# Performance work log

Hardware: AMD Instinct MI355X
Metric: run time of the kernel (lower is better)

## Reference

```python
import jax, jax.numpy as jnp
import numpy as np

D_MODEL = 512
NUM_HEADS = 8
DEPTH = D_MODEL // NUM_HEADS
B, S = 8, 1024


def setup_inputs() -> dict:
    key = jax.random.key(0)
    ks = jax.random.split(key, 14)
    scale = 1.0 / np.sqrt(D_MODEL)
    inp = {
        "q_in": jax.random.normal(ks[0], (B, S, D_MODEL), jnp.float32),
        "k_in": jax.random.normal(ks[1], (B, S, D_MODEL), jnp.float32),
        "v_in": jax.random.normal(ks[2], (B, S, D_MODEL), jnp.float32),
        # padding mask: 1 = masked-out position
        "mask": jax.random.randint(ks[3], (B, 1, 1, S), 0, 2).astype(jnp.float32),
        "additional_weights": jax.random.uniform(ks[4], (B, S, S), jnp.float32),
        "wq": jax.random.normal(ks[5], (D_MODEL, D_MODEL), jnp.float32) * scale,
        "bq": jnp.zeros((D_MODEL,), jnp.float32),
        "wk": jax.random.normal(ks[6], (D_MODEL, D_MODEL), jnp.float32) * scale,
        "bk": jnp.zeros((D_MODEL,), jnp.float32),
        "wv": jax.random.normal(ks[7], (D_MODEL, D_MODEL), jnp.float32) * scale,
        "bv": jnp.zeros((D_MODEL,), jnp.float32),
        "wo": jax.random.normal(ks[8], (D_MODEL, D_MODEL), jnp.float32) * scale,
        "bo": jnp.zeros((D_MODEL,), jnp.float32),
    }
    return inp


def _split_heads(x):
    # [B, S, d_model] -> [B, H, S, depth]
    b, s, _ = x.shape
    return x.reshape(b, s, NUM_HEADS, DEPTH).transpose(0, 2, 1, 3)


def reference(q_in, k_in, v_in, mask, additional_weights,
              wq, bq, wk, bk, wv, bv, wo, bo):
    q = _split_heads(q_in @ wq + bq)  # [B,H,S,D]
    k = _split_heads(k_in @ wk + bk)
    v = _split_heads(v_in @ wv + bv)

    scores = jnp.einsum("bhqd,bhkd->bhqk", q, k) / jnp.sqrt(
        jnp.asarray(DEPTH, q.dtype))
    scores = scores + mask * -1e9
    attn = jax.nn.softmax(scores, axis=-1)
    # post-softmax multiplicative weights, broadcast over heads
    attn = attn * additional_weights[:, None, :, :]
    x = jnp.einsum("bhqk,bhkd->bhqd", attn, v)
    x = x.transpose(0, 2, 1, 3).reshape(q_in.shape[0], -1, D_MODEL)
    out = x @ wo + bo
    return out, attn
```

## Files before the change

kernel.cpp:

```cpp
#include <hip/hip_runtime.h>
#include <stdint.h>

typedef unsigned short u16;
typedef short bf16x8 __attribute__((ext_vector_type(8)));
typedef float f32x4 __attribute__((ext_vector_type(4)));
typedef u16 u16x8 __attribute__((ext_vector_type(8)));

#define NHEADS 8
#define SEQ 1024
#define DM 512
#define DEPTH 64
#define BATCH 8
#define PSTRIDE 1032

__device__ __forceinline__ u16 f2bf(float f) {
    union { float f; unsigned u; } v; v.f = f;
    unsigned r = v.u + 0x7FFF + ((v.u >> 16) & 1);
    return (u16)(r >> 16);
}

__global__ void __launch_bounds__(256) transpose512(
    const float* __restrict__ w0, const float* __restrict__ w1,
    const float* __restrict__ w2, const float* __restrict__ w3,
    u16* __restrict__ wt)
{
    __shared__ float tile[32][33];
    const float* w = (blockIdx.z == 0) ? w0 : (blockIdx.z == 1) ? w1
                   : (blockIdx.z == 2) ? w2 : w3;
    u16* o = wt + (size_t)blockIdx.z * (DM * DM);
    int rb = blockIdx.y * 32, cb = blockIdx.x * 32;
    int tx = threadIdx.x, ty = threadIdx.y;
    #pragma unroll
    for (int k = 0; k < 32; k += 8)
        tile[ty + k][tx] = w[(size_t)(rb + ty + k) * DM + cb + tx];
    __syncthreads();
    #pragma unroll
    for (int k = 0; k < 32; k += 8)
        o[(size_t)(cb + ty + k) * DM + rb + tx] = f2bf(tile[tx][ty + k]);
}

__global__ void __launch_bounds__(256) conv_bf16(
    const float* __restrict__ q, const float* __restrict__ k,
    const float* __restrict__ v,
    u16* __restrict__ oq, u16* __restrict__ ok, u16* __restrict__ ov)
{
    const float* src = (blockIdx.z == 0) ? q : (blockIdx.z == 1) ? k : v;
    u16* dst = (blockIdx.z == 0) ? oq : (blockIdx.z == 1) ? ok : ov;
    size_t i = ((size_t)blockIdx.x * 256 + threadIdx.x) * 8;
    f32x4 a = *(const f32x4*)(src + i);
    f32x4 b = *(const f32x4*)(src + i + 4);
    u16x8 o;
    #pragma unroll
    for (int j = 0; j < 4; j++) { o[j] = f2bf(a[j]); o[j + 4] = f2bf(b[j]); }
    *(u16x8*)(dst + i) = o;
}

template <int LAYOUT>
__device__ __forceinline__ void gemm_tile(
    const u16* __restrict__ A, const u16* __restrict__ wt,
    const float* __restrict__ bias, void* __restrict__ out_)
{
    const int tid = threadIdx.x;
    const int wid = tid >> 6, lane = tid & 63;
    const int wm = wid >> 1, wn = wid & 1;
    const int mb = blockIdx.y * 128 + wm * 64;
    const int nb = blockIdx.x * 128 + wn * 64;
    const int lr = lane & 15, g = lane >> 4, lk = g * 8;

    f32x4 acc[4][4];
    #pragma unroll
    for (int i = 0; i < 4; i++)
        #pragma unroll
        for (int j = 0; j < 4; j++) acc[i][j] = (f32x4)0.f;

    for (int ks = 0; ks < DM; ks += 32) {
        bf16x8 a[4], bf[4];
        #pragma unroll
        for (int mt = 0; mt < 4; mt++)
            a[mt] = *(const bf16x8*)(A + (size_t)(mb + mt * 16 + lr) * DM + ks + lk);
        #pragma unroll
        for (int nt = 0; nt < 4; nt++)
            bf[nt] = *(const bf16x8*)(wt + (size_t)(nb + nt * 16 + lr) * DM + ks + lk);
        #pragma unroll
        for (int mt = 0; mt < 4; mt++)
            #pragma unroll
            for (int nt = 0; nt < 4; nt++) {
                if (LAYOUT == 1)
                    acc[mt][nt] = __builtin_amdgcn_mfma_f32_16x16x32_bf16(
                        bf[nt], a[mt], acc[mt][nt], 0, 0, 0);
                else
                    acc[mt][nt] = __builtin_amdgcn_mfma_f32_16x16x32_bf16(
                        a[mt], bf[nt], acc[mt][nt], 0, 0, 0);
            }
    }

    #pragma unroll
    for (int mt = 0; mt < 4; mt++) {
        #pragma unroll
        for (int nt = 0; nt < 4; nt++) {
            #pragma unroll
            for (int r = 0; r < 4; r++) {
                if (LAYOUT == 1) {
                    int m = mb + mt * 16 + lr;
                    int n = nb + nt * 16 + 4 * g + r;
                    float val = acc[mt][nt][r] + bias[n];
                    int b_ = m >> 10, s = m & 1023, h = n >> 6, d = n & 63;
                    ((u16*)out_)[((size_t)((b_ * NHEADS + h) << 6) + d) * SEQ + s] = f2bf(val);
                } else {
                    int n = nb + nt * 16 + lr;
                    int m = mb + mt * 16 + 4 * g + r;
                    float val = acc[mt][nt][r] + bias[n];
                    if (LAYOUT == 2) {
                        ((float*)out_)[(size_t)m * DM + n] = val;
                    } else {
                        int b_ = m >> 10, s = m & 1023, h = n >> 6, d = n & 63;
                        ((u16*)out_)[(((size_t)(b_ * NHEADS + h) * SEQ + s) << 6) + d] = f2bf(val);
                    }
                }
            }
        }
    }
}

__global__ void __launch_bounds__(256) qkv_proj(
    const u16* __restrict__ qbf, const u16* __restrict__ kbf,
    const u16* __restrict__ vbf, const u16* __restrict__ wt_base,
    const float* __restrict__ bq, const float* __restrict__ bk,
    const float* __restrict__ bv,
    u16* __restrict__ Qb, u16* __restrict__ Kb, u16* __restrict__ VTb)
{
    int z = blockIdx.z;
    if (z == 0)      gemm_tile<0>(qbf, wt_base,               bq, Qb);
    else if (z == 1) gemm_tile<0>(kbf, wt_base + DM * DM,     bk, Kb);
    else             gemm_tile<1>(vbf, wt_base + 2 * DM * DM, bv, VTb);
}

__global__ void __launch_bounds__(256) out_proj(
    const u16* __restrict__ X, const u16* __restrict__ wto,
    const float* __restrict__ bo, float* __restrict__ out)
{
    gemm_tile<2>(X, wto, bo, out);
}

__global__ void __launch_bounds__(256) attn_kernel(
    const u16* __restrict__ Q, const u16* __restrict__ K,
    const u16* __restrict__ VT, const float* __restrict__ mask,
    const float* __restrict__ addw, float* __restrict__ attn_out,
    u16* __restrict__ X)
{
    __shared__ u16 Pl[16 * PSTRIDE];
    __shared__ float redm[4][16];
    __shared__ float reds[4][16];
    const int h = blockIdx.x, qt = blockIdx.y, b = blockIdx.z;
    const int tid = threadIdx.x, wid = tid >> 6, lane = tid & 63;
    const int lr = lane & 15, g = lane >> 4, lk = g * 8;
    const size_t head = (size_t)(b * NHEADS + h) * (SEQ * DEPTH);
    const u16* Qh = Q + head + (size_t)qt * 16 * DEPTH;
    const u16* Kh = K + head;
    const u16* Vh = VT + head;
    const int cbase = (wid << 8) + lr;

    bf16x8 af0 = *(const bf16x8*)(Qh + lr * DEPTH + lk);
    bf16x8 af1 = *(const bf16x8*)(Qh + lr * DEPTH + 32 + lk);
    f32x4 acc[16];
    #pragma unroll
    for (int nt = 0; nt < 16; nt++) acc[nt] = (f32x4)0.f;
    #pragma unroll
    for (int nt = 0; nt < 16; nt++) {
        const u16* kp = Kh + (size_t)(cbase + (nt << 4)) * DEPTH + lk;
        bf16x8 b0 = *(const bf16x8*)kp;
        bf16x8 b1 = *(const bf16x8*)(kp + 32);
        acc[nt] = __builtin_amdgcn_mfma_f32_16x16x32_bf16(af0, b0, acc[nt], 0, 0, 0);
        acc[nt] = __builtin_amdgcn_mfma_f32_16x16x32_bf16(af1, b1, acc[nt], 0, 0, 0);
    }

    const float* mrow = mask + ((size_t)b << 10);
    float mx[4];
    #pragma unroll
    for (int r = 0; r < 4; r++) mx[r] = -3.0e38f;
    #pragma unroll
    for (int nt = 0; nt < 16; nt++) {
        float mp = mrow[cbase + (nt << 4)] * -1e9f;
        #pragma unroll
        for (int r = 0; r < 4; r++) {
            acc[nt][r] = acc[nt][r] * 0.125f + mp;
            mx[r] = fmaxf(mx[r], acc[nt][r]);
        }
    }
    #pragma unroll
    for (int off = 1; off < 16; off <<= 1)
        #pragma unroll
        for (int r = 0; r < 4; r++)
            mx[r] = fmaxf(mx[r], __shfl_xor(mx[r], off, 64));
    if (lr < 4)
        redm[wid][4 * g + lr] = (lr == 0) ? mx[0] : (lr == 1) ? mx[1]
                              : (lr == 2) ? mx[2] : mx[3];
    __syncthreads();
    float gm[4];
    #pragma unroll
    for (int r = 0; r < 4; r++)
        gm[r] = fmaxf(fmaxf(redm[0][4 * g + r], redm[1][4 * g + r]),
                      fmaxf(redm[2][4 * g + r], redm[3][4 * g + r]));

    float sm[4];
    #pragma unroll
    for (int r = 0; r < 4; r++) sm[r] = 0.f;
    #pragma unroll
    for (int nt = 0; nt < 16; nt++)
        #pragma unroll
        for (int r = 0; r < 4; r++) {
            float p = __expf(acc[nt][r] - gm[r]);
            acc[nt][r] = p;
            sm[r] += p;
        }
    #pragma unroll
    for (int off = 1; off < 16; off <<= 1)
        #pragma unroll
        for (int r = 0; r < 4; r++)
            sm[r] += __shfl_xor(sm[r], off, 64);
    if (lr < 4)
        reds[wid][4 * g + lr] = (lr == 0) ? sm[0] : (lr == 1) ? sm[1]
                              : (lr == 2) ? sm[2] : sm[3];
    __syncthreads();
    float iv[4];
    #pragma unroll
    for (int r = 0; r < 4; r++)
        iv[r] = 1.0f / (reds[0][4 * g + r] + reds[1][4 * g + r] +
                        reds[2][4 * g + r] + reds[3][4 * g + r]);

    const int qr0 = qt * 16 + 4 * g;
    size_t awr = ((size_t)((b << 10) + qr0) << 10);
    size_t aor = ((size_t)(((b * NHEADS + h) << 10) + qr0) << 10);
    #pragma unroll
    for (int nt = 0; nt < 16; nt++) {
        int col = cbase + (nt << 4);
        #pragma unroll
        for (int r = 0; r < 4; r++) {
            float val = acc[nt][r] * iv[r] * addw[awr + ((size_t)r << 10) + col];
            attn_out[aor + ((size_t)r << 10) + col] = val;
            Pl[(4 * g + r) * PSTRIDE + col] = f2bf(val);
        }
    }
    __syncthreads();

    f32x4 x = (f32x4)0.f;
    const u16* vrow = Vh + (size_t)((wid << 4) + lr) * SEQ;
    for (int ks = 0; ks < SEQ; ks += 32) {
        bf16x8 a = *(const bf16x8*)(Pl + lr * PSTRIDE + ks + lk);
        bf16x8 bv = *(const bf16x8*)(vrow + ks + lk);
        x = __builtin_amdgcn_mfma_f32_16x16x32_bf16(a, bv, x, 0, 0, 0);
    }
    int d = (h << 6) + (wid << 4) + lr;
    #pragma unroll
    for (int r = 0; r < 4; r++)
        X[((size_t)((b << 10) + qt * 16 + 4 * g + r)) * DM + d] = f2bf(x[r]);
}

extern "C" void kernel_launch(void* const* d_in, const int* in_sizes, int n_in,
                              void* d_out, int out_size, void* d_ws, size_t ws_size,
                              hipStream_t stream)
{
    const float* q_in = (const float*)d_in[0];
    const float* k_in = (const float*)d_in[1];
    const float* v_in = (const float*)d_in[2];
    const float* mask = (const float*)d_in[3];
    const float* addw = (const float*)d_in[4];
    const float* wq = (const float*)d_in[5];
    const float* bq = (const float*)d_in[6];
    const float* wk = (const float*)d_in[7];
    const float* bk = (const float*)d_in[8];
    const float* wv = (const float*)d_in[9];
    const float* bv = (const float*)d_in[10];
    const float* wo = (const float*)d_in[11];
    const float* bo = (const float*)d_in[12];

    const size_t ACT = (size_t)BATCH * SEQ * DM;

    u16* ws = (u16*)d_ws;
    u16* wt  = ws;
    u16* Qb  = wt + 4 * DM * DM;
    u16* Kb  = Qb + ACT;
    u16* VTb = Kb + ACT;
    u16* Xb  = VTb + ACT;

    float* out0 = (float*)d_out;
    float* attn_out = out0 + ACT;

    u16* qbf = (u16*)attn_out;
    u16* kbf = qbf + ACT;
    u16* vbf = kbf + ACT;

    transpose512<<<dim3(16, 16, 4), dim3(32, 8), 0, stream>>>(wq, wk, wv, wo, wt);
    conv_bf16<<<dim3(2048, 1, 3), 256, 0, stream>>>(q_in, k_in, v_in, qbf, kbf, vbf);
    qkv_proj<<<dim3(4, 64, 3), 256, 0, stream>>>(qbf, kbf, vbf, wt, bq, bk, bv,
                                                 Qb, Kb, VTb);
    attn_kernel<<<dim3(8, 64, 8), 256, 0, stream>>>(Qb, Kb, VTb, mask, addw,
                                                    attn_out, Xb);
    out_proj<<<dim3(4, 64, 1), 256, 0, stream>>>(Xb, wt + 3 * DM * DM, bo, out0);
}
```

Measured before the change: 578.8 us.

## Transpose QK^T MFMA operands for vectorized row-wise softmax stores and XCD-aware grid

Swaps the MFMA operand order so each lane holds four consecutive key columns of a single query row. The mask and additional-weights loads, the attn output stores and the LDS P writes can then be issued as 4-wide vectors instead of strided scalars. The cross-lane reductions shrink to two shuffles. The launch is flattened to a 1D grid with a remapping so that consecutive block IDs, which round-robin across XCDs, cover all heads of the same (b,qt); this is meant to improve L2 reuse of the additional-weights rows. The risk is LDS bank conflicts on the 4-wide P writes.

Result: no change. 582.6 us (+0.7%).

```diff
diff --git a/kernel.cpp b/kernel.cpp
--- a/kernel.cpp
+++ b/kernel.cpp
@@ -5,6 +5,7 @@
 typedef short bf16x8 __attribute__((ext_vector_type(8)));
 typedef float f32x4 __attribute__((ext_vector_type(4)));
 typedef u16 u16x8 __attribute__((ext_vector_type(8)));
+typedef u16 u16x4 __attribute__((ext_vector_type(4)));
 
 #define NHEADS 8
 #define SEQ 1024
@@ -151,95 +152,85 @@
     __shared__ u16 Pl[16 * PSTRIDE];
     __shared__ float redm[4][16];
     __shared__ float reds[4][16];
-    const int h = blockIdx.x, qt = blockIdx.y, b = blockIdx.z;
+
+    const int id = blockIdx.x;
+    const int c = id & 7, t = id >> 3;
+    const int h = t & 7;
+    const int p = ((t >> 3) << 3) | c;
+    const int qt = p & 63, b = p >> 6;
+
     const int tid = threadIdx.x, wid = tid >> 6, lane = tid & 63;
     const int lr = lane & 15, g = lane >> 4, lk = g * 8;
     const size_t head = (size_t)(b * NHEADS + h) * (SEQ * DEPTH);
     const u16* Qh = Q + head + (size_t)qt * 16 * DEPTH;
     const u16* Kh = K + head;
     const u16* Vh = VT + head;
-    const int cbase = (wid << 8) + lr;
-
-    bf16x8 af0 = *(const bf16x8*)(Qh + lr * DEPTH + lk);
-    bf16x8 af1 = *(const bf16x8*)(Qh + lr * DEPTH + 32 + lk);
+    const int wbase = wid << 8;
+
+    bf16x8 qf0 = *(const bf16x8*)(Qh + lr * DEPTH + lk);
+    bf16x8 qf1 = *(const bf16x8*)(Qh + lr * DEPTH + 32 + lk);
     f32x4 acc[16];
     #pragma unroll
     for (int nt = 0; nt < 16; nt++) acc[nt] = (f32x4)0.f;
     #pragma unroll
     for (int nt = 0; nt < 16; nt++) {
-        const u16* kp = Kh + (size_t)(cbase + (nt << 4)) * DEPTH + lk;
-        bf16x8 b0 = *(const bf16x8*)kp;
-        bf16x8 b1 = *(const bf16x8*)(kp + 32);
-        acc[nt] = __builtin_amdgcn_mfma_f32_16x16x32_bf16(af0, b0, acc[nt], 0, 0, 0);
-        acc[nt] = __builtin_amdgcn_mfma_f32_16x16x32_bf16(af1, b1, acc[nt], 0, 0, 0);
+        const u16* kp = Kh + (size_t)(wbase + (nt << 4) + lr) * DEPTH + lk;
+        bf16x8 k0 = *(const bf16x8*)kp;
+        bf16x8 k1 = *(const bf16x8*)(kp + 32);
+        acc[nt] = __builtin_amdgcn_mfma_f32_16x16x32_bf16(k0, qf0, acc[nt], 0, 0, 0);
+        acc[nt] = __builtin_amdgcn_mfma_f32_16x16x32_bf16(k1, qf1, acc[nt], 0, 0, 0);
     }
 
     const float* mrow = mask + ((size_t)b << 10);
-    float mx[4];
-    #pragma unroll
-    for (int r = 0; r < 4; r++) mx[r] = -3.0e38f;
+    float mx = -3.0e38f;
     #pragma unroll
     for (int nt = 0; nt < 16; nt++) {
-        float mp = mrow[cbase + (nt << 4)] * -1e9f;
+        f32x4 mr = *(const f32x4*)(mrow + wbase + (nt << 4) + 4 * g);
         #pragma unroll
         for (int r = 0; r < 4; r++) {
-            acc[nt][r] = acc[nt][r] * 0.125f + mp;
-            mx[r] = fmaxf(mx[r], acc[nt][r]);
-        }
-    }
-    #pragma unroll
-    for (int off = 1; off < 16; off <<= 1)
-        #pragma unroll
-        for (int r = 0; r < 4; r++)
-            mx[r] = fmaxf(mx[r], __shfl_xor(mx[r], off, 64));
-    if (lr < 4)
-        redm[wid][4 * g + lr] = (lr == 0) ? mx[0] : (lr == 1) ? mx[1]
-                              : (lr == 2) ? mx[2] : mx[3];
-    __syncthreads();
-    float gm[4];
-    #pragma unroll
-    for (int r = 0; r < 4; r++)
-        gm[r] = fmaxf(fmaxf(redm[0][4 * g + r], redm[1][4 * g + r]),
-                      fmaxf(redm[2][4 * g + r], redm[3][4 * g + r]));
-
-    float sm[4];
-    #pragma unroll
-    for (int r = 0; r < 4; r++) sm[r] = 0.f;
+            acc[nt][r] = acc[nt][r] * 0.125f + mr[r] * -1e9f;
+            mx = fmaxf(mx, acc[nt][r]);
+        }
+    }
+    mx = fmaxf(mx, __shfl_xor(mx, 16, 64));
+    mx = fmaxf(mx, __shfl_xor(mx, 32, 64));
+    if (lane < 16) redm[wid][lr] = mx;
+    __syncthreads();
+    float gm = fmaxf(fmaxf(redm[0][lr], redm[1][lr]),
+                     fmaxf(redm[2][lr], redm[3][lr]));
+
+    float sm = 0.f;
     #pragma unroll
     for (int nt = 0; nt < 16; nt++)
         #pragma unroll
         for (int r = 0; r < 4; r++) {
-            float p = __expf(acc[nt][r] - gm[r]);
-            acc[nt][r] = p;
-            sm[r] += p;
-        }
-    #pragma unroll
-    for (int off = 1; off < 16; off <<= 1)
-        #pragma unroll
-        for (int r = 0; r < 4; r++)
-            sm[r] += __shfl_xor(sm[r], off, 64);
-    if (lr < 4)
-        reds[wid][4 * g + lr] = (lr == 0) ? sm[0] : (lr == 1) ? sm[1]
-                              : (lr == 2) ? sm[2] : sm[3];
-    __syncthreads();
-    float iv[4];
-    #pragma unroll
-    for (int r = 0; r < 4; r++)
-        iv[r] = 1.0f / (reds[0][4 * g + r] + reds[1][4 * g + r] +
-                        reds[2][4 * g + r] + reds[3][4 * g + r]);
-
-    const int qr0 = qt * 16 + 4 * g;
-    size_t awr = ((size_t)((b << 10) + qr0) << 10);
-    size_t aor = ((size_t)(((b * NHEADS + h) << 10) + qr0) << 10);
+            float pv = __expf(acc[nt][r] - gm);
+            acc[nt][r] = pv;
+            sm += pv;
+        }
+    sm += __shfl_xor(sm, 16, 64);
+    sm += __shfl_xor(sm, 32, 64);
+    if (lane < 16) reds[wid][lr] = sm;
+    __syncthreads();
+    float iv = 1.0f / (reds[0][lr] + reds[1][lr] + reds[2][lr] + reds[3][lr]);
+
+    const int qglob = (qt << 4) + lr;
+    const size_t awbase = ((size_t)((b << 10) + qglob)) << 10;
+    const size_t aobase = ((size_t)(((b * NHEADS + h) << 10) + qglob)) << 10;
     #pragma unroll
     for (int nt = 0; nt < 16; nt++) {
-        int col = cbase + (nt << 4);
+        int k0 = wbase + (nt << 4) + 4 * g;
+        f32x4 aw = *(const f32x4*)(addw + awbase + k0);
+        f32x4 o;
+        u16x4 pb;
         #pragma unroll
         for (int r = 0; r < 4; r++) {
-            float val = acc[nt][r] * iv[r] * addw[awr + ((size_t)r << 10) + col];
-            attn_out[aor + ((size_t)r << 10) + col] = val;
-            Pl[(4 * g + r) * PSTRIDE + col] = f2bf(val);
-        }
+            float v = acc[nt][r] * iv * aw[r];
+            o[r] = v;
+            pb[r] = f2bf(v);
+        }
+        *(f32x4*)(attn_out + aobase + k0) = o;
+        *(u16x4*)(Pl + lr * PSTRIDE + k0) = pb;
     }
     __syncthreads();
 
@@ -253,7 +244,7 @@
     int d = (h << 6) + (wid << 4) + lr;
     #pragma unroll
     for (int r = 0; r < 4; r++)
-        X[((size_t)((b << 10) + qt * 16 + 4 * g + r)) * DM + d] = f2bf(x[r]);
+        X[((size_t)((b << 10) + (qt << 4) + 4 * g + r)) * DM + d] = f2bf(x[r]);
 }
 
 extern "C" void kernel_launch(void* const* d_in, const int* in_sizes, int n_in,
@@ -294,7 +285,7 @@
     conv_bf16<<<dim3(2048, 1, 3), 256, 0, stream>>>(q_in, k_in, v_in, qbf, kbf, vbf);
     qkv_proj<<<dim3(4, 64, 3), 256, 0, stream>>>(qbf, kbf, vbf, wt, bq, bk, bv,
                                                  Qb, Kb, VTb);
-    attn_kernel<<<dim3(8, 64, 8), 256, 0, stream>>>(Qb, Kb, VTb, mask, addw,
-                                                    attn_out, Xb);
+    attn_kernel<<<dim3(4096), 256, 0, stream>>>(Qb, Kb, VTb, mask, addw,
+                                                attn_out, Xb);
     out_proj<<<dim3(4, 64, 1), 256, 0, stream>>>(Xb, wt + 3 * DM * DM, bo, out0);
 }
```
